# Kernel tuning notes

Measured on AMD Instinct MI355X. Metric: run time of the kernel, lower is better.

Reference implementation:

```python
import jax, jax.numpy as jnp
import numpy as np

# --- config constants (from working_memory config) ---
R = 3.9; STRENGTH = 0.1; N_ITER = 10                      # logistic map
I0 = 1.0; OMEGA = 1.0; KWAVE = 2.0; ALPHA_BASE = 1.0      # Padilha wave
LC = 0.5; DE = 2.0; CHIRP_N = 1; AMIN = 0.1; AMAX = 3.0
FD = 1.5; T = 0.0                                          # fractal dim, time
ATT_ALPHA = 1.5; EPS = 1e-10                               # spectral filter
FCI = 0.7; STAB = 0.8; DEMAND = 0.6                        # neurotransmitter drives
BASE = 0.5; SENS = 1.0; DECAY = 0.1

B, S, D4 = 4, 2048, 1024  # batch, seq_len (= memory_size), embed_dim*4


def hamilton(a, b):
    # quaternion (Hamilton) product; last dim split into 4 component blocks
    aw, ax, ay, az = jnp.split(a, 4, axis=-1)
    bw, bx, by, bz = jnp.split(b, 4, axis=-1)
    w = aw * bw - ax * bx - ay * by - az * bz
    x = aw * bx + ax * bw + ay * bz - az * by
    y = aw * by - ax * bz + ay * bw + az * bx
    z = aw * bz + ax * by - ay * bx + az * bw
    return jnp.concatenate([w, x, y, z], axis=-1)


def setup_inputs() -> dict:
    key = jax.random.key(0)
    ks = jax.random.split(key, 8)
    sc = 0.02
    return {
        "query": jax.random.normal(ks[0], (B, S, D4), jnp.float32),
        "memory": jax.random.normal(ks[1], (B, S, D4), jnp.float32),
        "Wq": jax.random.normal(ks[2], (D4, D4), jnp.float32) * sc,
        "bq": jnp.zeros((D4,), jnp.float32),
        "Wk": jax.random.normal(ks[3], (D4, D4), jnp.float32) * sc,
        "bk": jnp.zeros((D4,), jnp.float32),
        "Wv": jax.random.normal(ks[4], (D4, D4), jnp.float32) * sc,
        "bv": jnp.zeros((D4,), jnp.float32),
    }


def reference(query, memory, Wq, bq, Wk, bk, Wv, bv):
    # 1) chaotic modulation of query (logistic map on sigmoid(||x||))
    s = jax.nn.sigmoid(jnp.linalg.norm(query, axis=-1))  # [B,S]
    for _ in range(N_ITER):
        s = R * s * (1.0 - s)
    q = query * (1.0 + STRENGTH * (s[..., None] - 0.5))

    # 2) Padilha wave modulation along sequence
    seq = q.shape[1]
    alpha = float(np.clip(ALPHA_BASE * (1.0 + LC * (FD - DE) / DE), AMIN, AMAX))
    beta = 2 * CHIRP_N + 1 - 2 * FD
    lam = jnp.arange(seq, dtype=q.dtype) / seq
    wave = I0 * jnp.sin(OMEGA * T + alpha * lam) * jnp.cos(OMEGA * T - KWAVE * lam + beta * lam ** 2)
    q = q * (1.0 + 0.1 * wave[None, :, None])

    # 3) neurotransmitter scalar modulation of memory (one decay step from baseline)
    dop = (1 - DECAY) * BASE + DECAY * jax.nn.sigmoid(jnp.float32(FCI * SENS))
    ser = (1 - DECAY) * BASE + DECAY * jax.nn.sigmoid(jnp.float32(STAB * SENS))
    nor = (1 - DECAY) * BASE + DECAY * jax.nn.sigmoid(jnp.float32(DEMAND * SENS))
    mem = memory * (0.4 * dop + 0.3 * ser + 0.3 * nor)

    # 4) quaternionic spectral attention
    Q = q @ Wq.T + bq
    K = mem @ Wk.T + bk
    V = mem @ Wv.T + bv
    Qf = jnp.fft.fft(Q, axis=-2)
    Kf = jnp.fft.fft(K, axis=-2)
    Vf = jnp.fft.fft(V, axis=-2)
    kidx = jnp.arange(seq, dtype=jnp.float32)
    filt = jnp.exp(1j * ATT_ALPHA * jnp.arctan(jnp.log(kidx + EPS)))[None, :, None]
    QK = hamilton(Qf * filt, Kf * filt)
    QKV = hamilton(QK, Vf * filt)
    attended = jnp.fft.ifft(QKV, axis=-2).real.astype(query.dtype)
    return attended
```

## Files before the change

### kernel.cpp

```cpp
#include <hip/hip_runtime.h>
#include <hip/hip_fp16.h>
#include <math.h>

#define S 2048
#define D4 1024
#define NB 4
#define HS 1026
#define TWOPI 6.283185307179586f

typedef __attribute__((ext_vector_type(8))) short bf16x8;
typedef __attribute__((ext_vector_type(4))) float f32x4;

__device__ __forceinline__ float2 cmul(float2 a, float2 b){
  return make_float2(a.x*b.x - a.y*b.y, a.x*b.y + a.y*b.x);
}
__device__ __forceinline__ float2 cadd(float2 a, float2 b){ return make_float2(a.x+b.x, a.y+b.y); }
__device__ __forceinline__ float2 csub(float2 a, float2 b){ return make_float2(a.x-b.x, a.y-b.y); }

__device__ __forceinline__ unsigned short f2bf(float f){
  unsigned int u = __builtin_bit_cast(unsigned int, f);
  unsigned int r = (u + 0x7FFFu + ((u >> 16) & 1u)) >> 16;
  return (unsigned short)r;
}
__device__ __forceinline__ float bf2f(unsigned short u){
  unsigned int x = (unsigned int)u << 16;
  return __builtin_bit_cast(float, x);
}

__device__ __forceinline__ void gld16(const unsigned short* g, unsigned short* l){
  __builtin_amdgcn_global_load_lds((const __attribute__((address_space(1))) unsigned int*)g,
                                   (__attribute__((address_space(3))) unsigned int*)l,
                                   16, 0, 0);
}

__device__ __forceinline__ float2 twf(const float* twr, const float* twi, int m){
  int mm = m & 1023;
  float s = (m & 1024) ? -1.f : 1.f;
  int p = mm + (mm >> 5);
  return make_float2(s * twr[p], s * twi[p]);
}

__device__ __forceinline__ void dft8_fwd(const float2 a[8], float2 o[8]){
  const float RH = 0.70710678118654752f;
  float2 b0 = cadd(a[0],a[4]), b1 = cadd(a[1],a[5]), b2 = cadd(a[2],a[6]), b3 = cadd(a[3],a[7]);
  float2 c0 = csub(a[0],a[4]);
  float2 t1 = csub(a[1],a[5]);
  float2 c1 = make_float2(RH*(t1.x + t1.y), RH*(t1.y - t1.x));
  float2 t2 = csub(a[2],a[6]);
  float2 c2 = make_float2(t2.y, -t2.x);
  float2 t3 = csub(a[3],a[7]);
  float2 c3 = make_float2(RH*(t3.y - t3.x), RH*(-(t3.x + t3.y)));
  float2 e0 = cadd(b0,b2), e1 = cadd(b1,b3);
  float2 f0 = csub(b0,b2);
  float2 f1t = csub(b1,b3); float2 f1 = make_float2(f1t.y, -f1t.x);
  o[0] = cadd(e0,e1); o[4] = csub(e0,e1);
  o[2] = cadd(f0,f1); o[6] = csub(f0,f1);
  float2 g0 = cadd(c0,c2), g1 = cadd(c1,c3);
  float2 h0 = csub(c0,c2);
  float2 h1t = csub(c1,c3); float2 h1 = make_float2(h1t.y, -h1t.x);
  o[1] = cadd(g0,g1); o[5] = csub(g0,g1);
  o[3] = cadd(h0,h1); o[7] = csub(h0,h1);
}

__device__ __forceinline__ void dft8_inv(const float2 a[8], float2 o[8]){
  const float RH = 0.70710678118654752f;
  float2 b0 = cadd(a[0],a[4]), b1 = cadd(a[1],a[5]), b2 = cadd(a[2],a[6]), b3 = cadd(a[3],a[7]);
  float2 c0 = csub(a[0],a[4]);
  float2 t1 = csub(a[1],a[5]);
  float2 c1 = make_float2(RH*(t1.x - t1.y), RH*(t1.y + t1.x));
  float2 t2 = csub(a[2],a[6]);
  float2 c2 = make_float2(-t2.y, t2.x);
  float2 t3 = csub(a[3],a[7]);
  float2 c3 = make_float2(RH*(-(t3.x + t3.y)), RH*(t3.x - t3.y));
  float2 e0 = cadd(b0,b2), e1 = cadd(b1,b3);
  float2 f0 = csub(b0,b2);
  float2 f1t = csub(b1,b3); float2 f1 = make_float2(-f1t.y, f1t.x);
  o[0] = cadd(e0,e1); o[4] = csub(e0,e1);
  o[2] = cadd(f0,f1); o[6] = csub(f0,f1);
  float2 g0 = cadd(c0,c2), g1 = cadd(c1,c3);
  float2 h0 = csub(c0,c2);
  float2 h1t = csub(c1,c3); float2 h1 = make_float2(-h1t.y, h1t.x);
  o[1] = cadd(g0,g1); o[5] = csub(g0,g1);
  o[3] = cadd(h0,h1); o[7] = csub(h0,h1);
}

__device__ __forceinline__ void dft4_fwd(const float2 a[4], float2 o[4]){
  float2 b0 = cadd(a[0],a[2]), b1 = cadd(a[1],a[3]);
  float2 c0 = csub(a[0],a[2]);
  float2 c1t = csub(a[1],a[3]); float2 c1 = make_float2(c1t.y, -c1t.x);
  o[0]=cadd(b0,b1); o[2]=csub(b0,b1); o[1]=cadd(c0,c1); o[3]=csub(c0,c1);
}
__device__ __forceinline__ void dft4_inv(const float2 a[4], float2 o[4]){
  float2 b0 = cadd(a[0],a[2]), b1 = cadd(a[1],a[3]);
  float2 c0 = csub(a[0],a[2]);
  float2 c1t = csub(a[1],a[3]); float2 c1 = make_float2(-c1t.y, c1t.x);
  o[0]=cadd(b0,b1); o[2]=csub(b0,b1); o[1]=cadd(c0,c1); o[3]=csub(c0,c1);
}

__global__ __launch_bounds__(256) void prep_kernel(float* __restrict__ scale,
                                                   float2* __restrict__ filt3,
                                                   float2* __restrict__ twg,
                                                   float alpha, float beta){
  int i = blockIdx.x * 256 + threadIdx.x;
  float lam = (float)i / (float)S;
  float w = sinf(alpha * lam) * cosf(-2.0f * lam + beta * lam * lam);
  scale[i] = 0.95f * (1.0f + 0.1f * w);
  float th = 1.5f * atanf(logf((float)i + 1e-10f));
  float sn, cs; sincosf(3.0f * th, &sn, &cs);
  filt3[i] = make_float2(cs * (1.0f / 2048.0f), sn * (1.0f / 2048.0f));
  if (i < 1024){
    float s2, c2; sincosf((float)i * (TWOPI / 2048.f), &s2, &c2);
    twg[i]        = make_float2(c2, -s2);
    twg[1024 + i] = make_float2(c2,  s2);
  }
}

__global__ __launch_bounds__(256) void convert_all(const float* __restrict__ q,
                                                   const float* __restrict__ mem,
                                                   const float* __restrict__ Wq,
                                                   const float* __restrict__ Wk,
                                                   const float* __restrict__ Wv,
                                                   unsigned short* __restrict__ XqB,
                                                   unsigned short* __restrict__ XmB,
                                                   unsigned short* __restrict__ Wall,
                                                   const float* __restrict__ scale,
                                                   float cmem){
  int bid = blockIdx.x;
  if (bid < 8192){
    size_t i = ((size_t)bid * 256 + threadIdx.x) * 4;
    int s = (int)((i / D4) % S);
    float scl = scale[s];
    float4 v = *(const float4*)&q[i];
    ushort4 o;
    o.x = f2bf(v.x * scl); o.y = f2bf(v.y * scl);
    o.z = f2bf(v.z * scl); o.w = f2bf(v.w * scl);
    *(ushort4*)&XqB[i] = o;
  } else if (bid < 16384){
    size_t i = ((size_t)(bid - 8192) * 256 + threadIdx.x) * 4;
    float4 v = *(const float4*)&mem[i];
    ushort4 o;
    o.x = f2bf(v.x * cmem); o.y = f2bf(v.y * cmem);
    o.z = f2bf(v.z * cmem); o.w = f2bf(v.w * cmem);
    *(ushort4*)&XmB[i] = o;
  } else {
    int r = bid - 16384;
    int tensor = r >> 10;
    const float* Wsrc = (tensor == 0) ? Wq : (tensor == 1 ? Wk : Wv);
    size_t i = ((size_t)(r & 1023) * 256 + threadIdx.x) * 4;
    float4 v = *(const float4*)&Wsrc[i];
    ushort4 o;
    o.x = f2bf(v.x); o.y = f2bf(v.y);
    o.z = f2bf(v.z); o.w = f2bf(v.w);
    *(ushort4*)&(Wall + (size_t)tensor * D4 * D4)[i] = o;
  }
}

#define TM 128
#define TN 128
#define TKK 64
__global__ __launch_bounds__(256) void mfma_gemm_all(const unsigned short* __restrict__ Wall,
                                                     const unsigned short* __restrict__ XqB,
                                                     const unsigned short* __restrict__ XmB,
                                                     const float* __restrict__ bq,
                                                     const float* __restrict__ bk,
                                                     const float* __restrict__ bv,
                                                     unsigned short* __restrict__ Xb){
  __shared__ unsigned short sA[2][TM * TKK];
  __shared__ unsigned short sB[2][TN * TKK];
  const int z = blockIdx.z;
  const int tensor = z >> 2, b = z & 3;
  const size_t TEN = (size_t)NB * D4 * S;
  const unsigned short* A = Wall + (size_t)tensor * D4 * D4;
  const unsigned short* B = (tensor == 0 ? XqB : XmB) + (size_t)b * S * D4;
  const float* bias = (tensor == 0) ? bq : (tensor == 1 ? bk : bv);
  unsigned short* dst = Xb + (size_t)tensor * TEN + (size_t)b * D4 * S;
  const int m0 = blockIdx.y * TM;
  const int n0 = blockIdx.x * TN;
  const int t = threadIdx.x;
  const int w = t >> 6, l = t & 63;
  const int sr = l >> 3;
  const int sc = ((l & 7) ^ sr) * 8;
  const int wr = (w >> 1) * 64;
  const int wc = (w & 1) * 64;
  const int l15 = l & 15, lh = l >> 4;
  const int co0 = ((lh     ^ (l15 & 7)) * 8);
  const int co1 = (((4+lh) ^ (l15 & 7)) * 8);

  const unsigned short* gA = A + (size_t)(m0 + w * 32 + sr) * D4 + sc;
  const unsigned short* gB = B + (size_t)(n0 + w * 32 + sr) * D4 + sc;

  f32x4 acc[4][4] = {};

#define STAGE(buf, k0) do { \
    _Pragma("unroll") \
    for (int i_ = 0; i_ < 4; ++i_){ \
      gld16(gA + (k0) + (size_t)(8 * i_) * D4, &sA[buf][w * 2048 + i_ * 512]); \
      gld16(gB + (k0) + (size_t)(8 * i_) * D4, &sB[buf][w * 2048 + i_ * 512]); \
    } \
  } while(0)

#define COMPUTE(buf) do { \
    bf16x8 bfr0[4], bfr1[4]; \
    _Pragma("unroll") \
    for (int j_ = 0; j_ < 4; ++j_){ \
      int rb = (wc + j_ * 16 + l15) * TKK; \
      bfr0[j_] = *(const bf16x8*)&sB[buf][rb + co0]; \
      bfr1[j_] = *(const bf16x8*)&sB[buf][rb + co1]; \
    } \
    _Pragma("unroll") \
    for (int i_ = 0; i_ < 4; ++i_){ \
      int ra = (wr + i_ * 16 + l15) * TKK; \
      bf16x8 af0 = *(const bf16x8*)&sA[buf][ra + co0]; \
      bf16x8 af1 = *(const bf16x8*)&sA[buf][ra + co1]; \
      _Pragma("unroll") \
      for (int j_ = 0; j_ < 4; ++j_){ \
        acc[i_][j_] = __builtin_amdgcn_mfma_f32_16x16x32_bf16(af0, bfr0[j_], acc[i_][j_], 0, 0, 0); \
        acc[i_][j_] = __builtin_amdgcn_mfma_f32_16x16x32_bf16(af1, bfr1[j_], acc[i_][j_], 0, 0, 0); \
      } \
    } \
  } while(0)

  STAGE(0, 0);
  __syncthreads();
  #pragma unroll 1
  for (int k0 = 0; k0 < 16; ++k0){
    if (k0 < 15) STAGE((k0 + 1) & 1, (k0 + 1) * TKK);
    COMPUTE(k0 & 1);
    __syncthreads();
  }

#undef STAGE
#undef COMPUTE

  #pragma unroll
  for (int i = 0; i < 4; ++i){
    int mbase = m0 + wr + i * 16 + lh * 4;
    #pragma unroll
    for (int r = 0; r < 4; ++r){
      float bi = bias[mbase + r];
      unsigned short* drow = dst + (size_t)(mbase + r) * S + n0 + wc + l15;
      #pragma unroll
      for (int j = 0; j < 4; ++j)
        drow[j * 16] = f2bf(acc[i][j][r] + bi);
    }
  }
}

__global__ __launch_bounds__(256) void fftfwd2(const unsigned short* __restrict__ src,
                                               const float2* __restrict__ twg,
                                               __half2* __restrict__ hs){
  __shared__ float zr[2112], zi[2112];
  __shared__ float twr[1056], twi[1056];
  const int t = threadIdx.x;
  #pragma unroll
  for (int q = 0; q < 4; ++q){
    int m = t + 256 * q;
    float2 wv = twg[m];
    int p = m + (m >> 5);
    twr[p] = wv.x; twi[p] = wv.y;
  }
  const unsigned short* col0 = src + (size_t)(2 * blockIdx.x) * S;
  const unsigned short* col1 = col0 + S;
  float2 v[8], o[8];
  #pragma unroll
  for (int j = 0; j < 8; ++j)
    v[j] = make_float2(bf2f(col0[t + 256 * j]), bf2f(col1[t + 256 * j]));
  dft8_fwd(v, o);
  #pragma unroll
  for (int j = 0; j < 8; ++j){ int x = 8 * t + j; zr[x + (x>>5)] = o[j].x; zi[x + (x>>5)] = o[j].y; }
  __syncthreads();
  {
    int k = t & 7;
    #pragma unroll
    for (int l = 0; l < 8; ++l){ int x = t + 256 * l; v[l] = make_float2(zr[x + (x>>5)], zi[x + (x>>5)]); }
    #pragma unroll
    for (int l = 1; l < 8; ++l) v[l] = cmul(v[l], twf(twr, twi, 32 * l * k));
    dft8_fwd(v, o);
    __syncthreads();
    int base = 8 * t - 7 * k;
    #pragma unroll
    for (int j = 0; j < 8; ++j){ int x = base + 8 * j; zr[x + (x>>5)] = o[j].x; zi[x + (x>>5)] = o[j].y; }
  }
  __syncthreads();
  {
    int k = t & 63;
    #pragma unroll
    for (int l = 0; l < 8; ++l){ int x = t + 256 * l; v[l] = make_float2(zr[x + (x>>5)], zi[x + (x>>5)]); }
    #pragma unroll
    for (int l = 1; l < 8; ++l) v[l] = cmul(v[l], twf(twr, twi, 4 * l * k));
    dft8_fwd(v, o);
    __syncthreads();
    int base = 8 * t - 7 * k;
    #pragma unroll
    for (int j = 0; j < 8; ++j){ int x = base + 64 * j; zr[x + (x>>5)] = o[j].x; zi[x + (x>>5)] = o[j].y; }
  }
  __syncthreads();
  {
    float2 a[4], oa[4], bb[4], ob[4];
    #pragma unroll
    for (int l = 0; l < 4; ++l){
      int xa = t + 512 * l;        a[l]  = make_float2(zr[xa + (xa>>5)], zi[xa + (xa>>5)]);
      int xb = t + 256 + 512 * l;  bb[l] = make_float2(zr[xb + (xb>>5)], zi[xb + (xb>>5)]);
    }
    #pragma unroll
    for (int l = 1; l < 4; ++l){
      a[l]  = cmul(a[l],  twf(twr, twi, l * t));
      bb[l] = cmul(bb[l], twf(twr, twi, l * (t + 256)));
    }
    dft4_fwd(a, oa); dft4_fwd(bb, ob);
    __syncthreads();
    #pragma unroll
    for (int j = 0; j < 4; ++j){
      int xa = t + 512 * j;        zr[xa + (xa>>5)] = oa[j].x; zi[xa + (xa>>5)] = oa[j].y;
      int xb = t + 256 + 512 * j;  zr[xb + (xb>>5)] = ob[j].x; zi[xb + (xb>>5)] = ob[j].y;
    }
  }
  __syncthreads();
  __half2* h0 = hs + (size_t)(2 * blockIdx.x) * HS;
  __half2* h1 = h0 + HS;
  #pragma unroll
  for (int q = 0; q < 4; ++q){
    int k = t + 256 * q;
    int km = (2048 - k) & 2047;
    float2 Zk = make_float2(zr[k + (k>>5)],  zi[k + (k>>5)]);
    float2 Zm = make_float2(zr[km + (km>>5)], zi[km + (km>>5)]);
    h0[k] = __float22half2_rn(make_float2(0.5f * (Zk.x + Zm.x), 0.5f * (Zk.y - Zm.y)));
    h1[k] = __float22half2_rn(make_float2(0.5f * (Zk.y + Zm.y), 0.5f * (Zm.x - Zk.x)));
  }
  if (t == 0){
    float2 Zk = make_float2(zr[1024 + (1024>>5)], zi[1024 + (1024>>5)]);
    h0[1024] = __float22half2_rn(make_float2(Zk.x, 0.f));
    h1[1024] = __float22half2_rn(make_float2(Zk.y, 0.f));
  }
}

__global__ __launch_bounds__(512) void hamifft3(const __half2* __restrict__ hs,
                                                const float2* __restrict__ filt3,
                                                const float2* __restrict__ twg,
                                                __half* __restrict__ oreal){
  __shared__ float2 h2s[4][1025];
  __shared__ float zr[2][2112], zi[2][2112];
  __shared__ float twr[1056], twi[1056];
  const int t = threadIdx.x;
  const int b = blockIdx.x >> 8;
  const int j = blockIdx.x & 255;
  #pragma unroll
  for (int q = 0; q < 2; ++q){
    int m = t + 512 * q;
    float2 wv = twg[m];
    int p = m + (m >> 5);
    twr[p] = wv.x; twi[p] = wv.y;
  }
  const size_t CH = (size_t)256 * HS;
  const size_t cQ = ((size_t)b * D4 + j) * HS;
  const size_t cK = cQ + (size_t)NB * D4 * HS;
  const size_t cV = cK + (size_t)NB * D4 * HS;
  for (int pass = 0; pass < 3; ++pass){
    int f;
    if (pass < 2) f = t + 512 * pass;
    else { if (t != 0) break; f = 1024; }
    float2 q0 = __half22float2(hs[cQ + f]),        q1 = __half22float2(hs[cQ + CH + f]),
           q2 = __half22float2(hs[cQ + 2*CH + f]), q3 = __half22float2(hs[cQ + 3*CH + f]);
    float2 k0 = __half22float2(hs[cK + f]),        k1 = __half22float2(hs[cK + CH + f]),
           k2 = __half22float2(hs[cK + 2*CH + f]), k3 = __half22float2(hs[cK + 3*CH + f]);
    float2 v0 = __half22float2(hs[cV + f]),        v1 = __half22float2(hs[cV + CH + f]),
           v2 = __half22float2(hs[cV + 2*CH + f]), v3 = __half22float2(hs[cV + 3*CH + f]);
    float2 hw = csub(csub(csub(cmul(q0,k0), cmul(q1,k1)), cmul(q2,k2)), cmul(q3,k3));
    float2 hx = csub(cadd(cadd(cmul(q0,k1), cmul(q1,k0)), cmul(q2,k3)), cmul(q3,k2));
    float2 hy = cadd(cadd(csub(cmul(q0,k2), cmul(q1,k3)), cmul(q2,k0)), cmul(q3,k1));
    float2 hz = csub(cadd(cadd(cmul(q0,k3), cmul(q1,k2)), cmul(q3,k0)), cmul(q2,k1));
    h2s[0][f] = csub(csub(csub(cmul(hw,v0), cmul(hx,v1)), cmul(hy,v2)), cmul(hz,v3));
    h2s[1][f] = csub(cadd(cadd(cmul(hw,v1), cmul(hx,v0)), cmul(hy,v3)), cmul(hz,v2));
    h2s[2][f] = cadd(cadd(csub(cmul(hw,v2), cmul(hx,v3)), cmul(hy,v0)), cmul(hz,v1));
    h2s[3][f] = csub(cadd(cadd(cmul(hw,v3), cmul(hx,v2)), cmul(hz,v0)), cmul(hy,v1));
  }
  __syncthreads();

  const int h = t >> 8;
  const int tt = t & 255;
  float* hzr = zr[h]; float* hzi = zi[h];
  for (int cc = 0; cc < 2; ++cc){
    const int c = 2 * cc + h;
    float2 v[8], o[8];
    #pragma unroll
    for (int q = 0; q < 8; ++q){
      int f = tt + 256 * q;
      float2 z;
      if (f <= 1024){
        z = cmul(h2s[c][f], filt3[f]);
      } else {
        float2 hv = h2s[c][2048 - f];
        z = cmul(make_float2(hv.x, -hv.y), filt3[f]);
      }
      v[q] = z;
    }
    dft8_inv(v, o);
    #pragma unroll
    for (int j2 = 0; j2 < 8; ++j2){ int x = 8 * tt + j2; hzr[x + (x>>5)] = o[j2].x; hzi[x + (x>>5)] = o[j2].y; }
    __syncthreads();
    {
      int k = tt & 7;
      #pragma unroll
      for (int l = 0; l < 8; ++l){ int x = tt + 256 * l; v[l] = make_float2(hzr[x + (x>>5)], hzi[x + (x>>5)]); }
      #pragma unroll
      for (int l = 1; l < 8; ++l) v[l] = cmul(v[l], twf(twr, twi, 32 * l * k));
      dft8_inv(v, o);
      __syncthreads();
      int base = 8 * tt - 7 * k;
      #pragma unroll
      for (int j2 = 0; j2 < 8; ++j2){ int x = base + 8 * j2; hzr[x + (x>>5)] = o[j2].x; hzi[x + (x>>5)] = o[j2].y; }
    }
    __syncthreads();
    {
      int k = tt & 63;
      #pragma unroll
      for (int l = 0; l < 8; ++l){ int x = tt + 256 * l; v[l] = make_float2(hzr[x + (x>>5)], hzi[x + (x>>5)]); }
      #pragma unroll
      for (int l = 1; l < 8; ++l) v[l] = cmul(v[l], twf(twr, twi, 4 * l * k));
      dft8_inv(v, o);
      __syncthreads();
      int base = 8 * tt - 7 * k;
      #pragma unroll
      for (int j2 = 0; j2 < 8; ++j2){ int x = base + 64 * j2; hzr[x + (x>>5)] = o[j2].x; hzi[x + (x>>5)] = o[j2].y; }
    }
    __syncthreads();
    {
      float2 a[4], oa[4], bb[4], ob[4];
      #pragma unroll
      for (int l = 0; l < 4; ++l){
        int xa = tt + 512 * l;        a[l]  = make_float2(hzr[xa + (xa>>5)], hzi[xa + (xa>>5)]);
        int xb = tt + 256 + 512 * l;  bb[l] = make_float2(hzr[xb + (xb>>5)], hzi[xb + (xb>>5)]);
      }
      #pragma unroll
      for (int l = 1; l < 4; ++l){
        a[l]  = cmul(a[l],  twf(twr, twi, l * tt));
        bb[l] = cmul(bb[l], twf(twr, twi, l * (tt + 256)));
      }
      dft4_inv(a, oa); dft4_inv(bb, ob);
      __syncthreads();
      #pragma unroll
      for (int j2 = 0; j2 < 4; ++j2){
        int xa = tt + 512 * j2;        hzr[xa + (xa>>5)] = oa[j2].x; hzi[xa + (xa>>5)] = oa[j2].y;
        int xb = tt + 256 + 512 * j2;  hzr[xb + (xb>>5)] = ob[j2].x; hzi[xb + (xb>>5)] = ob[j2].y;
      }
    }
    __syncthreads();
    __half* ocol = oreal + ((size_t)b * D4 + (j + 256 * c)) * S;
    #pragma unroll
    for (int q = 0; q < 8; ++q){
      int sx = tt + 256 * q;
      ocol[sx] = __float2half(hzr[sx + (sx>>5)]);
    }
    __syncthreads();
  }
}

__global__ __launch_bounds__(256) void transpose_kernel(const __half* __restrict__ src,
                                                        float* __restrict__ out){
  __shared__ float tile[32][33];
  const int b  = blockIdx.z;
  const int s0 = blockIdx.x * 32;
  const int d0 = blockIdx.y * 32;
  const int tx = threadIdx.x, ty = threadIdx.y;
  #pragma unroll
  for (int i = 0; i < 32; i += 8)
    tile[ty + i][tx] = __half2float(src[((size_t)(b * D4 + d0 + ty + i)) * S + (s0 + tx)]);
  __syncthreads();
  #pragma unroll
  for (int i = 0; i < 32; i += 8)
    out[((size_t)(b * S + s0 + ty + i)) * D4 + (d0 + tx)] = tile[tx][ty + i];
}

extern "C" void kernel_launch(void* const* d_in, const int* in_sizes, int n_in,
                              void* d_out, int out_size, void* d_ws, size_t ws_size,
                              hipStream_t stream){
  const float* query  = (const float*)d_in[0];
  const float* memory = (const float*)d_in[1];
  const float* Wq = (const float*)d_in[2];
  const float* bq = (const float*)d_in[3];
  const float* Wk = (const float*)d_in[4];
  const float* bk = (const float*)d_in[5];
  const float* Wv = (const float*)d_in[6];
  const float* bv = (const float*)d_in[7];
  float* out = (float*)d_out;

  const size_t TEN = (size_t)NB * D4 * S;
  unsigned short* Xb = (unsigned short*)d_ws;
  __half* oreal = (__half*)(Xb + 3 * TEN);
  float* wsScale = (float*)(oreal + TEN);
  float2* wsFilt3 = (float2*)(wsScale + S);
  float2* wsTwg   = wsFilt3 + S;
  char* A0 = (char*)(wsTwg + S);
  unsigned short* XqB  = (unsigned short*)A0;
  unsigned short* XmB  = XqB + TEN;
  unsigned short* Wall = XmB + TEN;
  __half2* hs = (__half2*)A0;

  double dop = 0.45 + 0.1 / (1.0 + exp(-0.7));
  double ser = 0.45 + 0.1 / (1.0 + exp(-0.8));
  double nor = 0.45 + 0.1 / (1.0 + exp(-0.6));
  float cmem = (float)(0.4 * dop + 0.3 * ser + 0.3 * nor);
  float alpha = 0.875f, beta = 0.0f;

  prep_kernel<<<8, 256, 0, stream>>>(wsScale, wsFilt3, wsTwg, alpha, beta);

  convert_all<<<19456, 256, 0, stream>>>(query, memory, Wq, Wk, Wv,
                                         XqB, XmB, Wall, wsScale, cmem);

  dim3 gg(S / TN, D4 / TM, 12);
  mfma_gemm_all<<<gg, 256, 0, stream>>>(Wall, XqB, XmB, bq, bk, bv, Xb);

  fftfwd2<<<3 * NB * D4 / 2, 256, 0, stream>>>(Xb, wsTwg, hs);

  hamifft3<<<NB * 256, 512, 0, stream>>>(hs, wsFilt3, wsTwg + 1024, oreal);

  dim3 tg(S / 32, D4 / 32, NB);
  transpose_kernel<<<tg, dim3(32, 8), 0, stream>>>(oreal, out);
}
```

Measured before the change: 170.2 us.

## Replace full-length inverse FFT with half-length complex-to-real inverse FFT

The inverse FFT in hamifft3 now folds the Hermitian spectrum into a 1024-point complex transform whose real and imaginary outputs are the even and odd real samples. It does this with a pre-twiddle and a combined filter (real part of the filter's even part), then runs five radix-4 stages. The aim is to halve the inverse FFT work and the shared memory it needs, and to write packed half2 outputs. In exchange it adds more synchronisation stages, and its correctness depends on the folded filter matching the real-part extraction.

```diff
diff --git a/kernel.cpp b/kernel.cpp
--- a/kernel.cpp
+++ b/kernel.cpp
@@ -62,28 +62,6 @@
   o[3] = cadd(h0,h1); o[7] = csub(h0,h1);
 }
 
-__device__ __forceinline__ void dft8_inv(const float2 a[8], float2 o[8]){
-  const float RH = 0.70710678118654752f;
-  float2 b0 = cadd(a[0],a[4]), b1 = cadd(a[1],a[5]), b2 = cadd(a[2],a[6]), b3 = cadd(a[3],a[7]);
-  float2 c0 = csub(a[0],a[4]);
-  float2 t1 = csub(a[1],a[5]);
-  float2 c1 = make_float2(RH*(t1.x - t1.y), RH*(t1.y + t1.x));
-  float2 t2 = csub(a[2],a[6]);
-  float2 c2 = make_float2(-t2.y, t2.x);
-  float2 t3 = csub(a[3],a[7]);
-  float2 c3 = make_float2(RH*(-(t3.x + t3.y)), RH*(t3.x - t3.y));
-  float2 e0 = cadd(b0,b2), e1 = cadd(b1,b3);
-  float2 f0 = csub(b0,b2);
-  float2 f1t = csub(b1,b3); float2 f1 = make_float2(-f1t.y, f1t.x);
-  o[0] = cadd(e0,e1); o[4] = csub(e0,e1);
-  o[2] = cadd(f0,f1); o[6] = csub(f0,f1);
-  float2 g0 = cadd(c0,c2), g1 = cadd(c1,c3);
-  float2 h0 = csub(c0,c2);
-  float2 h1t = csub(c1,c3); float2 h1 = make_float2(-h1t.y, h1t.x);
-  o[1] = cadd(g0,g1); o[5] = csub(g0,g1);
-  o[3] = cadd(h0,h1); o[7] = csub(h0,h1);
-}
-
 __device__ __forceinline__ void dft4_fwd(const float2 a[4], float2 o[4]){
   float2 b0 = cadd(a[0],a[2]), b1 = cadd(a[1],a[3]);
   float2 c0 = csub(a[0],a[2]);
@@ -98,16 +76,22 @@
 }
 
 __global__ __launch_bounds__(256) void prep_kernel(float* __restrict__ scale,
-                                                   float2* __restrict__ filt3,
+                                                   float2* __restrict__ gfilt,
                                                    float2* __restrict__ twg,
                                                    float alpha, float beta){
   int i = blockIdx.x * 256 + threadIdx.x;
   float lam = (float)i / (float)S;
   float w = sinf(alpha * lam) * cosf(-2.0f * lam + beta * lam * lam);
   scale[i] = 0.95f * (1.0f + 0.1f * w);
-  float th = 1.5f * atanf(logf((float)i + 1e-10f));
-  float sn, cs; sincosf(3.0f * th, &sn, &cs);
-  filt3[i] = make_float2(cs * (1.0f / 2048.0f), sn * (1.0f / 2048.0f));
+  if (i <= 1024){
+    int im = (2048 - i) & 2047;
+    float th1 = 1.5f * atanf(logf((float)i  + 1e-10f));
+    float th2 = 1.5f * atanf(logf((float)im + 1e-10f));
+    float s1, c1, s2, c2;
+    sincosf(3.0f * th1, &s1, &c1);
+    sincosf(3.0f * th2, &s2, &c2);
+    gfilt[i] = make_float2((c1 + c2) * (1.0f / 4096.0f), (s1 - s2) * (1.0f / 4096.0f));
+  }
   if (i < 1024){
     float s2, c2; sincosf((float)i * (TWOPI / 2048.f), &s2, &c2);
     twg[i]        = make_float2(c2, -s2);
@@ -335,11 +319,11 @@
 }
 
 __global__ __launch_bounds__(512) void hamifft3(const __half2* __restrict__ hs,
-                                                const float2* __restrict__ filt3,
+                                                const float2* __restrict__ gfilt,
                                                 const float2* __restrict__ twg,
                                                 __half* __restrict__ oreal){
   __shared__ float2 h2s[4][1025];
-  __shared__ float zr[2][2112], zi[2][2112];
+  __shared__ float zr[2][1056], zi[2][1056];
   __shared__ float twr[1056], twi[1056];
   const int t = threadIdx.x;
   const int b = blockIdx.x >> 8;
@@ -381,75 +365,42 @@
   float* hzr = zr[h]; float* hzi = zi[h];
   for (int cc = 0; cc < 2; ++cc){
     const int c = 2 * cc + h;
-    float2 v[8], o[8];
-    #pragma unroll
-    for (int q = 0; q < 8; ++q){
-      int f = tt + 256 * q;
-      float2 z;
-      if (f <= 1024){
-        z = cmul(h2s[c][f], filt3[f]);
-      } else {
-        float2 hv = h2s[c][2048 - f];
-        z = cmul(make_float2(hv.x, -hv.y), filt3[f]);
-      }
-      v[q] = z;
-    }
-    dft8_inv(v, o);
-    #pragma unroll
-    for (int j2 = 0; j2 < 8; ++j2){ int x = 8 * tt + j2; hzr[x + (x>>5)] = o[j2].x; hzi[x + (x>>5)] = o[j2].y; }
-    __syncthreads();
-    {
-      int k = tt & 7;
+    #pragma unroll
+    for (int q = 0; q < 4; ++q){
+      int k = tt + 256 * q;
+      float2 ya = cmul(h2s[c][k],        gfilt[k]);
+      float2 yb = cmul(h2s[c][1024 - k], gfilt[1024 - k]);
+      float2 ybc = make_float2(yb.x, -yb.y);
+      float2 e = cadd(ya, ybc);
+      float2 od = csub(ya, ybc);
+      float2 wv = twf(twr, twi, k);
+      float2 wo = cmul(wv, od);
+      zr[h][k + (k>>5)] = e.x - wo.y;
+      zi[h][k + (k>>5)] = e.y + wo.x;
+    }
+    __syncthreads();
+    #pragma unroll
+    for (int s = 0; s < 5; ++s){
+      const int p = 1 << (2 * s);
+      float2 a[4], o4[4];
       #pragma unroll
-      for (int l = 0; l < 8; ++l){ int x = tt + 256 * l; v[l] = make_float2(hzr[x + (x>>5)], hzi[x + (x>>5)]); }
+      for (int l = 0; l < 4; ++l){ int x = tt + 256 * l; a[l] = make_float2(hzr[x + (x>>5)], hzi[x + (x>>5)]); }
+      int k = tt & (p - 1);
+      int mstep = k * (512 / p);
       #pragma unroll
-      for (int l = 1; l < 8; ++l) v[l] = cmul(v[l], twf(twr, twi, 32 * l * k));
-      dft8_inv(v, o);
+      for (int l = 1; l < 4; ++l) a[l] = cmul(a[l], twf(twr, twi, l * mstep));
+      dft4_inv(a, o4);
       __syncthreads();
-      int base = 8 * tt - 7 * k;
+      int base = 4 * tt - 3 * k;
       #pragma unroll
-      for (int j2 = 0; j2 < 8; ++j2){ int x = base + 8 * j2; hzr[x + (x>>5)] = o[j2].x; hzi[x + (x>>5)] = o[j2].y; }
-    }
-    __syncthreads();
-    {
-      int k = tt & 63;
-      #pragma unroll
-      for (int l = 0; l < 8; ++l){ int x = tt + 256 * l; v[l] = make_float2(hzr[x + (x>>5)], hzi[x + (x>>5)]); }
-      #pragma unroll
-      for (int l = 1; l < 8; ++l) v[l] = cmul(v[l], twf(twr, twi, 4 * l * k));
-      dft8_inv(v, o);
+      for (int j2 = 0; j2 < 4; ++j2){ int x = base + j2 * p; hzr[x + (x>>5)] = o4[j2].x; hzi[x + (x>>5)] = o4[j2].y; }
       __syncthreads();
-      int base = 8 * tt - 7 * k;
-      #pragma unroll
-      for (int j2 = 0; j2 < 8; ++j2){ int x = base + 64 * j2; hzr[x + (x>>5)] = o[j2].x; hzi[x + (x>>5)] = o[j2].y; }
-    }
-    __syncthreads();
-    {
-      float2 a[4], oa[4], bb[4], ob[4];
-      #pragma unroll
-      for (int l = 0; l < 4; ++l){
-        int xa = tt + 512 * l;        a[l]  = make_float2(hzr[xa + (xa>>5)], hzi[xa + (xa>>5)]);
-        int xb = tt + 256 + 512 * l;  bb[l] = make_float2(hzr[xb + (xb>>5)], hzi[xb + (xb>>5)]);
-      }
-      #pragma unroll
-      for (int l = 1; l < 4; ++l){
-        a[l]  = cmul(a[l],  twf(twr, twi, l * tt));
-        bb[l] = cmul(bb[l], twf(twr, twi, l * (tt + 256)));
-      }
-      dft4_inv(a, oa); dft4_inv(bb, ob);
-      __syncthreads();
-      #pragma unroll
-      for (int j2 = 0; j2 < 4; ++j2){
-        int xa = tt + 512 * j2;        hzr[xa + (xa>>5)] = oa[j2].x; hzi[xa + (xa>>5)] = oa[j2].y;
-        int xb = tt + 256 + 512 * j2;  hzr[xb + (xb>>5)] = ob[j2].x; hzi[xb + (xb>>5)] = ob[j2].y;
-      }
-    }
-    __syncthreads();
-    __half* ocol = oreal + ((size_t)b * D4 + (j + 256 * c)) * S;
-    #pragma unroll
-    for (int q = 0; q < 8; ++q){
-      int sx = tt + 256 * q;
-      ocol[sx] = __float2half(hzr[sx + (sx>>5)]);
+    }
+    __half2* ocol2 = (__half2*)(oreal + ((size_t)b * D4 + (j + 256 * c)) * S);
+    #pragma unroll
+    for (int q = 0; q < 4; ++q){
+      int n = tt + 256 * q;
+      ocol2[n] = __float22half2_rn(make_float2(hzr[n + (n>>5)], hzi[n + (n>>5)]));
     }
     __syncthreads();
   }
@@ -488,8 +439,8 @@
   unsigned short* Xb = (unsigned short*)d_ws;
   __half* oreal = (__half*)(Xb + 3 * TEN);
   float* wsScale = (float*)(oreal + TEN);
-  float2* wsFilt3 = (float2*)(wsScale + S);
-  float2* wsTwg   = wsFilt3 + S;
+  float2* wsGfilt = (float2*)(wsScale + S);
+  float2* wsTwg   = wsGfilt + S;
   char* A0 = (char*)(wsTwg + S);
   unsigned short* XqB  = (unsigned short*)A0;
   unsigned short* XmB  = XqB + TEN;
@@ -502,7 +453,7 @@
   float cmem = (float)(0.4 * dop + 0.3 * ser + 0.3 * nor);
   float alpha = 0.875f, beta = 0.0f;
 
-  prep_kernel<<<8, 256, 0, stream>>>(wsScale, wsFilt3, wsTwg, alpha, beta);
+  prep_kernel<<<8, 256, 0, stream>>>(wsScale, wsGfilt, wsTwg, alpha, beta);
 
   convert_all<<<19456, 256, 0, stream>>>(query, memory, Wq, Wk, Wv,
                                          XqB, XmB, Wall, wsScale, cmem);
@@ -512,7 +463,7 @@
 
   fftfwd2<<<3 * NB * D4 / 2, 256, 0, stream>>>(Xb, wsTwg, hs);
 
-  hamifft3<<<NB * 256, 512, 0, stream>>>(hs, wsFilt3, wsTwg + 1024, oreal);
+  hamifft3<<<NB * 256, 512, 0, stream>>>(hs, wsGfilt, wsTwg + 1024, oreal);
 
   dim3 tg(S / 32, D4 / 32, NB);
   transpose_kernel<<<tg, dim3(32, 8), 0, stream>>>(oreal, out);
```

Result: faster. 158.9 us (-6.6%).
